# Performance work log

Measured on AMD Instinct MI355X. Metric: run time of the kernel, lower is better.

## Reference

```python
import jax, jax.numpy as jnp
import numpy as np

N_EMBD = 1024
N_HEAD = 16
B, T = 4, 2048
EPS = 1e-5


def setup_inputs() -> dict:
    key = jax.random.key(0)
    ks = jax.random.split(key, 12)
    s = 0.02
    d, dff = N_EMBD, 4 * N_EMBD
    return {
        "x": jax.random.normal(ks[0], (B, T, d), dtype=jnp.float32),
        "ln1_w": jnp.ones((d,), jnp.float32),
        "ln1_b": jnp.zeros((d,), jnp.float32),
        "ln2_w": jnp.ones((d,), jnp.float32),
        "ln2_b": jnp.zeros((d,), jnp.float32),
        "w_attn": jax.random.normal(ks[1], (d, 3 * d), jnp.float32) * s,
        "b_attn": jnp.zeros((3 * d,), jnp.float32),
        "w_proj": jax.random.normal(ks[2], (d, d), jnp.float32) * s,
        "b_proj": jnp.zeros((d,), jnp.float32),
        "w_fc": jax.random.normal(ks[3], (d, dff), jnp.float32) * s,
        "b_fc": jnp.zeros((dff,), jnp.float32),
        "w_fc2": jax.random.normal(ks[4], (dff, d), jnp.float32) * s,
        "b_fc2": jnp.zeros((d,), jnp.float32),
    }


def _layernorm(x, w, b):
    mu = jnp.mean(x, axis=-1, keepdims=True)
    var = jnp.mean(jnp.square(x - mu), axis=-1, keepdims=True)
    return (x - mu) * jax.lax.rsqrt(var + EPS) * w + b


def reference(x, ln1_w, ln1_b, ln2_w, ln2_b, w_attn, b_attn, w_proj, b_proj,
              w_fc, b_fc, w_fc2, b_fc2):
    Bx, Tx, C = x.shape
    hd = C // N_HEAD
    # --- attention branch ---
    h = _layernorm(x, ln1_w, ln1_b)
    qkv = h @ w_attn + b_attn  # [B,T,3C]
    q, k, v = jnp.split(qkv, 3, axis=-1)
    q = q.reshape(Bx, Tx, N_HEAD, hd).transpose(0, 2, 1, 3)  # [B,H,T,hd]
    k = k.reshape(Bx, Tx, N_HEAD, hd).transpose(0, 2, 1, 3)
    v = v.reshape(Bx, Tx, N_HEAD, hd).transpose(0, 2, 1, 3)
    att = jnp.einsum("bhqd,bhkd->bhqk", q, k) * (1.0 / np.sqrt(hd))
    causal = jnp.tril(jnp.ones((Tx, Tx), dtype=bool))
    att = jnp.where(causal[None, None], att, -jnp.inf)
    att = jax.nn.softmax(att, axis=-1)
    y = jnp.einsum("bhqk,bhkd->bhqd", att, v)
    y = y.transpose(0, 2, 1, 3).reshape(Bx, Tx, C)
    x = x + (y @ w_proj + b_proj)
    # --- mlp branch ---
    h2 = _layernorm(x, ln2_w, ln2_b)
    m = jax.nn.gelu(h2 @ w_fc + b_fc, approximate=False)
    x = x + (m @ w_fc2 + b_fc2)
    return x
```

## Files before the change

kernel.cpp:

```cpp
#include <hip/hip_runtime.h>
#include <hip/hip_bf16.h>
#include <math.h>

typedef __bf16 bf16;
typedef __bf16 bf16x4 __attribute__((ext_vector_type(4)));
typedef __bf16 bf16x8 __attribute__((ext_vector_type(8)));
typedef float f32x4 __attribute__((ext_vector_type(4)));

__device__ __forceinline__ void gload_lds16(const bf16* g, bf16* l) {
  __builtin_amdgcn_global_load_lds(
      (const __attribute__((address_space(1))) void*)g,
      (__attribute__((address_space(3))) void*)l, 16, 0, 0);
}

#define MF(a, b, c) __builtin_amdgcn_mfma_f32_16x16x32_bf16((a), (b), (c), 0, 0, 0)
#define VM4_BAR()  asm volatile("s_waitcnt vmcnt(4)\ns_barrier" ::: "memory")
#define VM2_BAR()  asm volatile("s_waitcnt vmcnt(2)\ns_barrier" ::: "memory")
#define VM0_BAR()  asm volatile("s_waitcnt vmcnt(0)\ns_barrier" ::: "memory")
#define LGK0_SB()  do { asm volatile("s_waitcnt lgkmcnt(0)" ::: "memory"); \
                        __builtin_amdgcn_sched_barrier(0); } while (0)

template <int EPI, int KSPLIT>
__global__ __launch_bounds__(512, 2)
void gemmq(const bf16* __restrict__ A, const bf16* __restrict__ BT,
           const float* __restrict__ bias, const float* __restrict__ res,
           void* __restrict__ Cout, void* __restrict__ Cout2,
           int M, int N, int K)
{
  __shared__ alignas(16) bf16 lsA[2][16384];
  __shared__ alignas(16) bf16 lsB[2][16384];

  int nbn = N >> 8;
  int nwg = (M >> 8) * nbn;
  int bid = blockIdx.x;
  int ks = 0;
  if (KSPLIT == 2) { ks = (bid >= nwg) ? 1 : 0; bid -= ks * nwg; }
  int cpx = nwg >> 3;
  int wg  = (bid & 7) * cpx + (bid >> 3);
  int m0 = (wg / nbn) << 8;
  int n0 = (wg % nbn) << 8;

  int t = threadIdx.x;
  int l = t & 63, w = t >> 6;
  int wr = (w >> 2) << 6;
  int wc = (w & 3) << 5;
  int lr = l & 15, lg = l >> 4;

  int kb0 = (KSPLIT == 2) ? ks * (K >> 1) : 0;
  int nt = (K / KSPLIT) >> 6;

  const bf16* Ag = A  + (size_t)m0 * K + kb0;
  const bf16* Bg = BT + (size_t)n0 * K + kb0;

  int swz0 = (lg ^ (lr & 7)) << 3;
  int swz1 = swz0 ^ 32;
  int aRow = (wr + lr) << 6;
  int bRow = (wc + lr) << 6;

  const bf16* srcA[2]; const bf16* srcB[2];
#pragma unroll
  for (int j = 0; j < 2; ++j) {
    int ci = j * 512 + t;
    int r = ci >> 3;
    int g = (ci & 7) ^ (r & 7);
    srcA[j] = Ag + (size_t)r * K + g * 8;
    srcB[j] = Bg + (size_t)r * K + g * 8;
  }
  size_t qA = (size_t)128 * K;

#define STAGE_A(q, kofs, db) do { \
  _Pragma("unroll") \
  for (int j = 0; j < 2; ++j) \
    gload_lds16(srcA[j] + (q) * qA + (kofs), &lsA[db][(q) * 8192 + (j * 512 + t) * 8]); \
} while (0)
#define STAGE_B(q, kofs, db) do { \
  _Pragma("unroll") \
  for (int j = 0; j < 2; ++j) \
    gload_lds16(srcB[j] + (q) * qA + (kofs), &lsB[db][(q) * 8192 + (j * 512 + t) * 8]); \
} while (0)

  f32x4 acc[2][2][4][2];
  f32x4 zero = {0.f, 0.f, 0.f, 0.f};
#pragma unroll
  for (int qa = 0; qa < 2; ++qa)
#pragma unroll
    for (int qb = 0; qb < 2; ++qb)
#pragma unroll
      for (int mi = 0; mi < 4; ++mi)
#pragma unroll
        for (int ni = 0; ni < 2; ++ni) acc[qa][qb][mi][ni] = zero;

  STAGE_A(0, 0, 0);
  STAGE_B(0, 0, 0);
  STAGE_B(1, 0, 0);
  STAGE_A(1, 0, 0);

  bf16x8 afr[4][2], bfr0[2][2], bfr1[2][2];

  for (int T = 0; T < nt; ++T) {
    int c = T & 1, d = c ^ 1;
    bool st = (T + 1 < nt);
    int k64 = (T + 1) << 6;
    const bf16* pa = &lsA[c][0];
    const bf16* pb = &lsB[c][0];

    VM4_BAR();
#pragma unroll
    for (int mi = 0; mi < 4; ++mi) {
      afr[mi][0] = *(const bf16x8*)(pa + aRow + mi * 1024 + swz0);
      afr[mi][1] = *(const bf16x8*)(pa + aRow + mi * 1024 + swz1);
    }
#pragma unroll
    for (int ni = 0; ni < 2; ++ni) {
      bfr0[ni][0] = *(const bf16x8*)(pb + bRow + ni * 1024 + swz0);
      bfr0[ni][1] = *(const bf16x8*)(pb + bRow + ni * 1024 + swz1);
    }
    if (st) STAGE_A(0, k64, d);
    LGK0_SB();
    __builtin_amdgcn_s_setprio(1);
#pragma unroll
    for (int mi = 0; mi < 4; ++mi)
#pragma unroll
      for (int ni = 0; ni < 2; ++ni)
#pragma unroll
        for (int kk = 0; kk < 2; ++kk)
          acc[0][0][mi][ni] = MF(afr[mi][kk], bfr0[ni][kk], acc[0][0][mi][ni]);
    __builtin_amdgcn_s_setprio(0);

    if (st) VM4_BAR(); else VM2_BAR();
#pragma unroll
    for (int ni = 0; ni < 2; ++ni) {
      bfr1[ni][0] = *(const bf16x8*)(pb + 8192 + bRow + ni * 1024 + swz0);
      bfr1[ni][1] = *(const bf16x8*)(pb + 8192 + bRow + ni * 1024 + swz1);
    }
    if (st) STAGE_B(0, k64, d);
    LGK0_SB();
    __builtin_amdgcn_s_setprio(1);
#pragma unroll
    for (int mi = 0; mi < 4; ++mi)
#pragma unroll
      for (int ni = 0; ni < 2; ++ni)
#pragma unroll
        for (int kk = 0; kk < 2; ++kk)
          acc[0][1][mi][ni] = MF(afr[mi][kk], bfr1[ni][kk], acc[0][1][mi][ni]);
    __builtin_amdgcn_s_setprio(0);

    if (st) VM4_BAR(); else VM0_BAR();
#pragma unroll
    for (int mi = 0; mi < 4; ++mi) {
      afr[mi][0] = *(const bf16x8*)(pa + 8192 + aRow + mi * 1024 + swz0);
      afr[mi][1] = *(const bf16x8*)(pa + 8192 + aRow + mi * 1024 + swz1);
    }
    if (st) STAGE_B(1, k64, d);
    LGK0_SB();
    __builtin_amdgcn_s_setprio(1);
#pragma unroll
    for (int mi = 0; mi < 4; ++mi)
#pragma unroll
      for (int ni = 0; ni < 2; ++ni)
#pragma unroll
        for (int kk = 0; kk < 2; ++kk)
          acc[1][1][mi][ni] = MF(afr[mi][kk], bfr1[ni][kk], acc[1][1][mi][ni]);
    __builtin_amdgcn_s_setprio(0);

    if (st) STAGE_A(1, k64, d);
    __builtin_amdgcn_s_setprio(1);
#pragma unroll
    for (int mi = 0; mi < 4; ++mi)
#pragma unroll
      for (int ni = 0; ni < 2; ++ni)
#pragma unroll
        for (int kk = 0; kk < 2; ++kk)
          acc[1][0][mi][ni] = MF(afr[mi][kk], bfr0[ni][kk], acc[1][0][mi][ni]);
    __builtin_amdgcn_s_setprio(0);
  }

  const float SCLQ = 0.18033688011112042f;
  bf16* Pb = (bf16*)((KSPLIT == 2 && ks) ? Cout2 : Cout);
#pragma unroll
  for (int qa = 0; qa < 2; ++qa)
#pragma unroll
    for (int mi = 0; mi < 4; ++mi) {
      int row = m0 + qa * 128 + wr + mi * 16 + lg * 4;
#pragma unroll
      for (int qb = 0; qb < 2; ++qb)
#pragma unroll
        for (int ni = 0; ni < 2; ++ni) {
          int col = n0 + qb * 128 + wc + ni * 16 + lr;
          float bv = (EPI == 3) ? 0.f : bias[col];
          f32x4 a = acc[qa][qb][mi][ni];
#pragma unroll
          for (int r = 0; r < 4; ++r) {
            float v = a[r] + bv;
            size_t idx = (size_t)(row + r) * N + col;
            if (EPI == 0)      Pb[idx] = (bf16)v;
            else if (EPI == 1) ((float*)Cout)[idx] = v + res[idx];
            else if (EPI == 2) Pb[idx] = (bf16)(0.5f * v * (1.f + erff(v * 0.70710678118654752f)));
            else if (EPI == 4) Pb[idx] = (bf16)((col < 1024) ? v * SCLQ : v);
            else               Pb[idx] = (bf16)v;
          }
        }
    }
#undef STAGE_A
#undef STAGE_B
}

__global__ __launch_bounds__(256)
void combine2(const bf16* __restrict__ p0, const bf16* __restrict__ p1,
              const float* __restrict__ bias, const float* __restrict__ res,
              float* __restrict__ out)
{
  int i = (blockIdx.x * 256 + threadIdx.x) * 8;
  bf16x8 a = *(const bf16x8*)(p0 + i);
  bf16x8 b = *(const bf16x8*)(p1 + i);
  int c = i & 1023;
#pragma unroll
  for (int j = 0; j < 8; ++j)
    out[i + j] = (float)a[j] + (float)b[j] + bias[c + j] + res[i + j];
}

__global__ __launch_bounds__(256)
void combine_ln(const bf16* __restrict__ p0, const bf16* __restrict__ p1,
                const float* __restrict__ bias, const float* __restrict__ res,
                const float* __restrict__ lnw, const float* __restrict__ lnb,
                float* __restrict__ x1, bf16* __restrict__ hout)
{
  int row = blockIdx.x;
  int t = threadIdx.x;
  size_t i0 = (size_t)row * 1024 + t * 4;
  bf16x4 a = *(const bf16x4*)(p0 + i0);
  bf16x4 b = *(const bf16x4*)(p1 + i0);
  float4 r = *(const float4*)(res + i0);
  float4 bi = ((const float4*)bias)[t];
  float v0 = (float)a[0] + (float)b[0] + bi.x + r.x;
  float v1 = (float)a[1] + (float)b[1] + bi.y + r.y;
  float v2 = (float)a[2] + (float)b[2] + bi.z + r.z;
  float v3 = (float)a[3] + (float)b[3] + bi.w + r.w;
  float4 vv = {v0, v1, v2, v3};
  *(float4*)(x1 + i0) = vv;
  float s  = v0 + v1 + v2 + v3;
  float sq = v0 * v0 + v1 * v1 + v2 * v2 + v3 * v3;
#pragma unroll
  for (int off = 32; off >= 1; off >>= 1) {
    s  += __shfl_xor(s, off);
    sq += __shfl_xor(sq, off);
  }
  __shared__ float ps[4], pq[4];
  if ((t & 63) == 0) { ps[t >> 6] = s; pq[t >> 6] = sq; }
  __syncthreads();
  s  = ps[0] + ps[1] + ps[2] + ps[3];
  sq = pq[0] + pq[1] + pq[2] + pq[3];
  float mu  = s * (1.f / 1024.f);
  float var = sq * (1.f / 1024.f) - mu * mu;
  float rstd = rsqrtf(var + 1e-5f);
  float4 wv = ((const float4*)lnw)[t];
  float4 bv = ((const float4*)lnb)[t];
  hout[i0 + 0] = (bf16)((v0 - mu) * rstd * wv.x + bv.x);
  hout[i0 + 1] = (bf16)((v1 - mu) * rstd * wv.y + bv.y);
  hout[i0 + 2] = (bf16)((v2 - mu) * rstd * wv.z + bv.z);
  hout[i0 + 3] = (bf16)((v3 - mu) * rstd * wv.w + bv.w);
}

__global__ __launch_bounds__(256)
void ln_bf16(const float* __restrict__ x, const float* __restrict__ w,
             const float* __restrict__ b, bf16* __restrict__ out)
{
  int row = blockIdx.x;
  int t = threadIdx.x;
  float4 v = ((const float4*)(x + (size_t)row * 1024))[t];
  float s  = v.x + v.y + v.z + v.w;
  float sq = v.x * v.x + v.y * v.y + v.z * v.z + v.w * v.w;
#pragma unroll
  for (int off = 32; off >= 1; off >>= 1) {
    s  += __shfl_xor(s, off);
    sq += __shfl_xor(sq, off);
  }
  __shared__ float ps[4], pq[4];
  if ((t & 63) == 0) { ps[t >> 6] = s; pq[t >> 6] = sq; }
  __syncthreads();
  s  = ps[0] + ps[1] + ps[2] + ps[3];
  sq = pq[0] + pq[1] + pq[2] + pq[3];
  float mu  = s * (1.f / 1024.f);
  float var = sq * (1.f / 1024.f) - mu * mu;
  float rstd = rsqrtf(var + 1e-5f);
  float4 wv = ((const float4*)w)[t];
  float4 bv = ((const float4*)b)[t];
  size_t o0 = (size_t)row * 1024 + t * 4;
  out[o0 + 0] = (bf16)((v.x - mu) * rstd * wv.x + bv.x);
  out[o0 + 1] = (bf16)((v.y - mu) * rstd * wv.y + bv.y);
  out[o0 + 2] = (bf16)((v.z - mu) * rstd * wv.z + bv.z);
  out[o0 + 3] = (bf16)((v.w - mu) * rstd * wv.w + bv.w);
}

__global__ __launch_bounds__(256)
void transpose_cast(const float* __restrict__ W, bf16* __restrict__ WT, int K, int N)
{
  __shared__ float tile[32][33];
  int bk = blockIdx.x * 32, bn = blockIdx.y * 32;
  int tx = threadIdx.x & 31, ty = threadIdx.x >> 5;
#pragma unroll
  for (int i = ty; i < 32; i += 8)
    tile[i][tx] = W[(size_t)(bk + i) * N + bn + tx];
  __syncthreads();
#pragma unroll
  for (int i = ty; i < 32; i += 8)
    WT[(size_t)(bn + i) * K + bk + tx] = (bf16)tile[tx][i];
}

__global__ __launch_bounds__(256)
void vtrans(const bf16* __restrict__ qkv, bf16* __restrict__ vt)
{
  __shared__ alignas(16) bf16 tile[64 * 64];
  int bh = blockIdx.x;
  int b = bh >> 4, h = bh & 15;
  int t0 = blockIdx.y * 64;
  int t = threadIdx.x;
#pragma unroll
  for (int i = 0; i < 2; ++i) {
    int c = i * 256 + t;
    int tt = c >> 3, d8 = c & 7;
    bf16x8 v = *(const bf16x8*)(qkv + (size_t)(b * 2048 + t0 + tt) * 3072 + 2048 + h * 64 + d8 * 8);
    *(bf16x8*)&tile[(tt * 8 + (d8 ^ (tt >> 3))) * 8] = v;
  }
  __syncthreads();
#pragma unroll
  for (int i = 0; i < 2; ++i) {
    int c = i * 256 + t;
    int d = c >> 3, tt8 = c & 7;
    bf16x8 o;
#pragma unroll
    for (int j = 0; j < 8; ++j) {
      int row = tt8 * 8 + j;
      o[j] = tile[(row * 8 + ((d >> 3) ^ (row >> 3))) * 8 + (d & 7)];
    }
    *(bf16x8*)(vt + (size_t)(bh * 64 + d) * 2048 + t0 + tt8 * 8) = o;
  }
}

__global__ __launch_bounds__(512)
void attn_flash(const bf16* __restrict__ qkv, const bf16* __restrict__ vt,
                bf16* __restrict__ y)
{
  __shared__ alignas(16) bf16 lk[2][4096];
  __shared__ alignas(16) bf16 lv[2][4096];
  __shared__ alignas(16) bf16 lp[8][16 * 64];

  int bid = blockIdx.x;
  int bh = bid & 63;
  int qb = 15 - (bid >> 6);
  int b = bh >> 4, h = bh & 15;
  int t = threadIdx.x;
  int w = t >> 6, l = t & 63;
  int lr = l & 15, lg = l >> 4;
  int q0 = qb * 128;
  int qw = q0 + w * 16;
  const size_t RS = 3072;

  const bf16* qbase = qkv + (size_t)(b * 2048) * RS + h * 64;
  const bf16* kbase = qkv + (size_t)(b * 2048) * RS + 1024 + h * 64;
  const bf16* vtb   = vt + (size_t)(bh * 64) * 2048;

  bf16x8 qf[2];
#pragma unroll
  for (int kk = 0; kk < 2; ++kk)
    qf[kk] = *(const bf16x8*)(qbase + (size_t)(qw + lr) * RS + kk * 32 + lg * 8);

  int row = t >> 3, c8 = t & 7;
  int sc8 = c8 ^ (row & 7);
  const bf16* pK = kbase + (size_t)row * RS + sc8 * 8;
  const bf16* pV = vtb + (size_t)row * 2048 + sc8 * 8;
  int dst = t * 8;

  f32x4 zero = {0.f, 0.f, 0.f, 0.f};
  f32x4 o[4];
#pragma unroll
  for (int ni = 0; ni < 4; ++ni) o[ni] = zero;
  float lo[4] = {0.f, 0.f, 0.f, 0.f};

  int nkb = 2 * qb + 2;
  gload_lds16(pK, &lk[0][dst]);
  gload_lds16(pV, &lv[0][dst]);

  for (int kb = 0; kb < nkb; ++kb) {
    int cur = kb & 1;
    int k0 = kb * 64;
    VM0_BAR();
    if (kb + 1 < nkb) {
      pK += 64 * RS;
      pV += 64;
      gload_lds16(pK, &lk[cur ^ 1][dst]);
      gload_lds16(pV, &lv[cur ^ 1][dst]);
    }

    f32x4 s[4];
#pragma unroll
    for (int j = 0; j < 4; ++j) s[j] = zero;
#pragma unroll
    for (int kk = 0; kk < 2; ++kk)
#pragma unroll
      for (int j = 0; j < 4; ++j) {
        int krow = j * 16 + lr;
        bf16x8 kf = *(const bf16x8*)&lk[cur][krow * 64 + (((4 * kk + lg) ^ (krow & 7)) * 8)];
        s[j] = MF(qf[kk], kf, s[j]);
      }

    bool needmask = (k0 + 63 > qw);
    float p[4][4];
#pragma unroll
    for (int r = 0; r < 4; ++r) {
      int tq = qw + lg * 4 + r;
#pragma unroll
      for (int j = 0; j < 4; ++j) {
        float v = s[j][r];
        if (needmask && (k0 + j * 16 + lr > tq)) v = -1e30f;
        p[j][r] = exp2f(v);
      }
      lo[r] += (p[0][r] + p[1][r]) + (p[2][r] + p[3][r]);
    }

#pragma unroll
    for (int r = 0; r < 4; ++r) {
      int qr = lg * 4 + r;
#pragma unroll
      for (int j = 0; j < 4; ++j) {
        int ch = (2 * j + (lr >> 3)) ^ (qr & 7);
        lp[w][qr * 64 + ch * 8 + (lr & 7)] = (bf16)p[j][r];
      }
    }
    bf16x8 pa[2];
#pragma unroll
    for (int kf = 0; kf < 2; ++kf)
      pa[kf] = *(const bf16x8*)&lp[w][lr * 64 + (((4 * kf + lg) ^ (lr & 7)) * 8)];

#pragma unroll
    for (int ni = 0; ni < 4; ++ni)
#pragma unroll
      for (int kf = 0; kf < 2; ++kf) {
        int d = ni * 16 + lr;
        bf16x8 vf = *(const bf16x8*)&lv[cur][d * 64 + (((4 * kf + lg) ^ (d & 7)) * 8)];
        o[ni] = MF(pa[kf], vf, o[ni]);
      }
  }

#pragma unroll
  for (int r = 0; r < 4; ++r) {
#pragma unroll
    for (int off = 1; off < 16; off <<= 1) lo[r] += __shfl_xor(lo[r], off);
    lo[r] = 1.f / lo[r];
  }
#pragma unroll
  for (int ni = 0; ni < 4; ++ni)
#pragma unroll
    for (int r = 0; r < 4; ++r) {
      int tq = qw + lg * 4 + r;
      y[(size_t)(b * 2048 + tq) * 1024 + h * 64 + ni * 16 + lr] = (bf16)(o[ni][r] * lo[r]);
    }
}

extern "C" void kernel_launch(void* const* d_in, const int* in_sizes, int n_in,
                              void* d_out, int out_size, void* d_ws, size_t ws_size,
                              hipStream_t stream) {
  (void)in_sizes; (void)n_in; (void)out_size; (void)ws_size;
  const float* x      = (const float*)d_in[0];
  const float* ln1w   = (const float*)d_in[1];
  const float* ln1b   = (const float*)d_in[2];
  const float* ln2w   = (const float*)d_in[3];
  const float* ln2b   = (const float*)d_in[4];
  const float* w_attn = (const float*)d_in[5];
  const float* b_attn = (const float*)d_in[6];
  const float* w_proj = (const float*)d_in[7];
  const float* b_proj = (const float*)d_in[8];
  const float* w_fc   = (const float*)d_in[9];
  const float* b_fc   = (const float*)d_in[10];
  const float* w_fc2  = (const float*)d_in[11];
  const float* b_fc2  = (const float*)d_in[12];
  float* out = (float*)d_out;

  char* p = (char*)d_ws;
  bf16*  h     = (bf16*)p;  p += (size_t)8192 * 1024 * 2;
  bf16*  qkv   = (bf16*)p;
  bf16*  mbuf  = (bf16*)p;  p += (size_t)8192 * 3072 * 2;
  bf16*  ybuf  = (bf16*)p;  p += (size_t)8192 * 1024 * 2;
  float* x1    = (float*)p; p += (size_t)8192 * 1024 * 4;
  bf16*  wqkvT = (bf16*)p;  p += (size_t)3072 * 1024 * 2;
  bf16*  wprojT= (bf16*)p;  p += (size_t)1024 * 1024 * 2;
  bf16*  wfcT  = (bf16*)p;  p += (size_t)4096 * 1024 * 2;
  bf16*  wfc2T = (bf16*)p;  p += (size_t)1024 * 4096 * 2;
  bf16*  vt    = (bf16*)x1;
  bf16*  pp0   = qkv;
  bf16*  pp1   = qkv + (size_t)8192 * 1024;
  bf16*  sp0   = h;
  bf16*  sp1   = wqkvT;

  transpose_cast<<<dim3(1024 / 32, 3072 / 32), 256, 0, stream>>>(w_attn, wqkvT, 1024, 3072);
  transpose_cast<<<dim3(1024 / 32, 1024 / 32), 256, 0, stream>>>(w_proj, wprojT, 1024, 1024);
  transpose_cast<<<dim3(1024 / 32, 4096 / 32), 256, 0, stream>>>(w_fc,   wfcT,  1024, 4096);
  transpose_cast<<<dim3(4096 / 32, 1024 / 32), 256, 0, stream>>>(w_fc2,  wfc2T, 4096, 1024);

  ln_bf16<<<8192, 256, 0, stream>>>(x, ln1w, ln1b, h);
  gemmq<4, 1><<<384, 512, 0, stream>>>(h, wqkvT, b_attn, nullptr, qkv, nullptr, 8192, 3072, 1024);
  vtrans<<<dim3(64, 32), 256, 0, stream>>>(qkv, vt);
  attn_flash<<<1024, 512, 0, stream>>>(qkv, vt, ybuf);
  gemmq<3, 2><<<256, 512, 0, stream>>>(ybuf, wprojT, nullptr, nullptr, pp0, pp1, 8192, 1024, 1024);
  combine_ln<<<8192, 256, 0, stream>>>(pp0, pp1, b_proj, x, ln2w, ln2b, x1, h);
  gemmq<2, 1><<<512, 512, 0, stream>>>(h, wfcT, b_fc, nullptr, mbuf, nullptr, 8192, 4096, 1024);
  gemmq<3, 2><<<256, 512, 0, stream>>>(mbuf, wfc2T, nullptr, nullptr, sp0, sp1, 8192, 1024, 4096);
  combine2<<<4096, 256, 0, stream>>>(sp0, sp1, b_fc2, x1, out);
}
```

Before: 410.9 us.

## Software-pipeline LDS fragment loads across K tiles with register double-buffering

Restructures the GEMM main loop so the first A/B fragments for the next K tile are read from LDS at the end of the current tile, into a second set of registers. The loop is unrolled by two to alternate between the buffer sets. The explicit lgkmcnt(0) waits are replaced by scheduling fences, and the vmcnt thresholds are retuned to the new staging order. This aims to hide LDS read latency behind MFMA work and remove one barrier phase per tile. In exchange it adds VGPR pressure under a 512x2 launch bound, which could cause spills, and it assumes the tile count nt is even.

```diff
diff --git a/kernel.cpp b/kernel.cpp
--- a/kernel.cpp
+++ b/kernel.cpp
@@ -17,8 +17,7 @@
 #define VM4_BAR()  asm volatile("s_waitcnt vmcnt(4)\ns_barrier" ::: "memory")
 #define VM2_BAR()  asm volatile("s_waitcnt vmcnt(2)\ns_barrier" ::: "memory")
 #define VM0_BAR()  asm volatile("s_waitcnt vmcnt(0)\ns_barrier" ::: "memory")
-#define LGK0_SB()  do { asm volatile("s_waitcnt lgkmcnt(0)" ::: "memory"); \
-                        __builtin_amdgcn_sched_barrier(0); } while (0)
+#define SFENCE()   __builtin_amdgcn_sched_barrier(0)
 
 template <int EPI, int KSPLIT>
 __global__ __launch_bounds__(512, 2)
@@ -72,11 +71,13 @@
   _Pragma("unroll") \
   for (int j = 0; j < 2; ++j) \
     gload_lds16(srcA[j] + (q) * qA + (kofs), &lsA[db][(q) * 8192 + (j * 512 + t) * 8]); \
+  SFENCE(); \
 } while (0)
 #define STAGE_B(q, kofs, db) do { \
   _Pragma("unroll") \
   for (int j = 0; j < 2; ++j) \
     gload_lds16(srcB[j] + (q) * qA + (kofs), &lsB[db][(q) * 8192 + (j * 512 + t) * 8]); \
+  SFENCE(); \
 } while (0)
 
   f32x4 acc[2][2][4][2];
@@ -94,85 +95,102 @@
   STAGE_B(0, 0, 0);
   STAGE_B(1, 0, 0);
   STAGE_A(1, 0, 0);
-
-  bf16x8 afr[4][2], bfr0[2][2], bfr1[2][2];
-
-  for (int T = 0; T < nt; ++T) {
-    int c = T & 1, d = c ^ 1;
-    bool st = (T + 1 < nt);
-    int k64 = (T + 1) << 6;
-    const bf16* pa = &lsA[c][0];
-    const bf16* pb = &lsB[c][0];
-
-    VM4_BAR();
-#pragma unroll
-    for (int mi = 0; mi < 4; ++mi) {
-      afr[mi][0] = *(const bf16x8*)(pa + aRow + mi * 1024 + swz0);
-      afr[mi][1] = *(const bf16x8*)(pa + aRow + mi * 1024 + swz1);
-    }
-#pragma unroll
-    for (int ni = 0; ni < 2; ++ni) {
-      bfr0[ni][0] = *(const bf16x8*)(pb + bRow + ni * 1024 + swz0);
-      bfr0[ni][1] = *(const bf16x8*)(pb + bRow + ni * 1024 + swz1);
-    }
-    if (st) STAGE_A(0, k64, d);
-    LGK0_SB();
-    __builtin_amdgcn_s_setprio(1);
-#pragma unroll
-    for (int mi = 0; mi < 4; ++mi)
-#pragma unroll
-      for (int ni = 0; ni < 2; ++ni)
-#pragma unroll
-        for (int kk = 0; kk < 2; ++kk)
-          acc[0][0][mi][ni] = MF(afr[mi][kk], bfr0[ni][kk], acc[0][0][mi][ni]);
-    __builtin_amdgcn_s_setprio(0);
-
-    if (st) VM4_BAR(); else VM2_BAR();
-#pragma unroll
-    for (int ni = 0; ni < 2; ++ni) {
-      bfr1[ni][0] = *(const bf16x8*)(pb + 8192 + bRow + ni * 1024 + swz0);
-      bfr1[ni][1] = *(const bf16x8*)(pb + 8192 + bRow + ni * 1024 + swz1);
-    }
-    if (st) STAGE_B(0, k64, d);
-    LGK0_SB();
-    __builtin_amdgcn_s_setprio(1);
-#pragma unroll
-    for (int mi = 0; mi < 4; ++mi)
-#pragma unroll
-      for (int ni = 0; ni < 2; ++ni)
-#pragma unroll
-        for (int kk = 0; kk < 2; ++kk)
-          acc[0][1][mi][ni] = MF(afr[mi][kk], bfr1[ni][kk], acc[0][1][mi][ni]);
-    __builtin_amdgcn_s_setprio(0);
-
-    if (st) VM4_BAR(); else VM0_BAR();
-#pragma unroll
-    for (int mi = 0; mi < 4; ++mi) {
-      afr[mi][0] = *(const bf16x8*)(pa + 8192 + aRow + mi * 1024 + swz0);
-      afr[mi][1] = *(const bf16x8*)(pa + 8192 + aRow + mi * 1024 + swz1);
-    }
-    if (st) STAGE_B(1, k64, d);
-    LGK0_SB();
-    __builtin_amdgcn_s_setprio(1);
-#pragma unroll
-    for (int mi = 0; mi < 4; ++mi)
-#pragma unroll
-      for (int ni = 0; ni < 2; ++ni)
-#pragma unroll
-        for (int kk = 0; kk < 2; ++kk)
-          acc[1][1][mi][ni] = MF(afr[mi][kk], bfr1[ni][kk], acc[1][1][mi][ni]);
-    __builtin_amdgcn_s_setprio(0);
-
-    if (st) STAGE_A(1, k64, d);
-    __builtin_amdgcn_s_setprio(1);
-#pragma unroll
-    for (int mi = 0; mi < 4; ++mi)
-#pragma unroll
-      for (int ni = 0; ni < 2; ++ni)
-#pragma unroll
-        for (int kk = 0; kk < 2; ++kk)
-          acc[1][0][mi][ni] = MF(afr[mi][kk], bfr0[ni][kk], acc[1][0][mi][ni]);
-    __builtin_amdgcn_s_setprio(0);
+  VM4_BAR();
+
+  bf16x8 a0A[4][2], a0B[4][2], b0A[2][2], b0B[2][2];
+  bf16x8 afr1[4][2], bfr1[2][2];
+
+#pragma unroll
+  for (int mi = 0; mi < 4; ++mi) {
+    a0A[mi][0] = *(const bf16x8*)(&lsA[0][0] + aRow + mi * 1024 + swz0);
+    a0A[mi][1] = *(const bf16x8*)(&lsA[0][0] + aRow + mi * 1024 + swz1);
+  }
+#pragma unroll
+  for (int ni = 0; ni < 2; ++ni) {
+    b0A[ni][0] = *(const bf16x8*)(&lsB[0][0] + bRow + ni * 1024 + swz0);
+    b0A[ni][1] = *(const bf16x8*)(&lsB[0][0] + bRow + ni * 1024 + swz1);
+  }
+
+#define TILE_BODY(TT, CB, A0C, B0C, A0N, B0N) do { \
+  const bf16* pa = &lsA[CB][0]; \
+  const bf16* pb = &lsB[CB][0]; \
+  const int DB = (CB) ^ 1; \
+  bool st = ((TT) + 1 < nt); \
+  int k64 = ((TT) + 1) << 6; \
+   \
+  VM2_BAR(); \
+  _Pragma("unroll") \
+  for (int ni = 0; ni < 2; ++ni) { \
+    bfr1[ni][0] = *(const bf16x8*)(pb + 8192 + bRow + ni * 1024 + swz0); \
+    bfr1[ni][1] = *(const bf16x8*)(pb + 8192 + bRow + ni * 1024 + swz1); \
+  } \
+  if (st) STAGE_A(0, k64, DB); \
+  __builtin_amdgcn_s_setprio(1); \
+  _Pragma("unroll") \
+  for (int mi = 0; mi < 4; ++mi) \
+    _Pragma("unroll") \
+    for (int ni = 0; ni < 2; ++ni) \
+      _Pragma("unroll") \
+      for (int kk = 0; kk < 2; ++kk) \
+        acc[0][0][mi][ni] = MF(A0C[mi][kk], B0C[ni][kk], acc[0][0][mi][ni]); \
+  __builtin_amdgcn_s_setprio(0); \
+   \
+  if (st) VM2_BAR(); else VM0_BAR(); \
+  _Pragma("unroll") \
+  for (int mi = 0; mi < 4; ++mi) { \
+    afr1[mi][0] = *(const bf16x8*)(pa + 8192 + aRow + mi * 1024 + swz0); \
+    afr1[mi][1] = *(const bf16x8*)(pa + 8192 + aRow + mi * 1024 + swz1); \
+  } \
+  if (st) STAGE_B(0, k64, DB); \
+  __builtin_amdgcn_s_setprio(1); \
+  _Pragma("unroll") \
+  for (int mi = 0; mi < 4; ++mi) \
+    _Pragma("unroll") \
+    for (int ni = 0; ni < 2; ++ni) \
+      _Pragma("unroll") \
+      for (int kk = 0; kk < 2; ++kk) \
+        acc[0][1][mi][ni] = MF(A0C[mi][kk], bfr1[ni][kk], acc[0][1][mi][ni]); \
+  __builtin_amdgcn_s_setprio(0); \
+   \
+  if (st) STAGE_B(1, k64, DB); \
+  __builtin_amdgcn_s_setprio(1); \
+  _Pragma("unroll") \
+  for (int mi = 0; mi < 4; ++mi) \
+    _Pragma("unroll") \
+    for (int ni = 0; ni < 2; ++ni) \
+      _Pragma("unroll") \
+      for (int kk = 0; kk < 2; ++kk) \
+        acc[1][1][mi][ni] = MF(afr1[mi][kk], bfr1[ni][kk], acc[1][1][mi][ni]); \
+  __builtin_amdgcn_s_setprio(0); \
+   \
+  if (st) { \
+    VM2_BAR(); \
+    _Pragma("unroll") \
+    for (int mi = 0; mi < 4; ++mi) { \
+      A0N[mi][0] = *(const bf16x8*)(&lsA[DB][0] + aRow + mi * 1024 + swz0); \
+      A0N[mi][1] = *(const bf16x8*)(&lsA[DB][0] + aRow + mi * 1024 + swz1); \
+    } \
+    _Pragma("unroll") \
+    for (int ni = 0; ni < 2; ++ni) { \
+      B0N[ni][0] = *(const bf16x8*)(&lsB[DB][0] + bRow + ni * 1024 + swz0); \
+      B0N[ni][1] = *(const bf16x8*)(&lsB[DB][0] + bRow + ni * 1024 + swz1); \
+    } \
+    STAGE_A(1, k64, DB); \
+  } \
+  __builtin_amdgcn_s_setprio(1); \
+  _Pragma("unroll") \
+  for (int mi = 0; mi < 4; ++mi) \
+    _Pragma("unroll") \
+    for (int ni = 0; ni < 2; ++ni) \
+      _Pragma("unroll") \
+      for (int kk = 0; kk < 2; ++kk) \
+        acc[1][0][mi][ni] = MF(afr1[mi][kk], B0C[ni][kk], acc[1][0][mi][ni]); \
+  __builtin_amdgcn_s_setprio(0); \
+} while (0)
+
+  for (int T = 0; T < nt; T += 2) {
+    TILE_BODY(T,     0, a0A, b0A, a0B, b0B);
+    TILE_BODY(T + 1, 1, a0B, b0B, a0A, b0A);
   }
 
   const float SCLQ = 0.18033688011112042f;
@@ -203,6 +221,7 @@
     }
 #undef STAGE_A
 #undef STAGE_B
+#undef TILE_BODY
 }
 
 __global__ __launch_bounds__(256)
```

After: 997.5 us. 2.43x slower.

## Prefetch next k-tile fragments into registers at end of GEMM iteration

Applied to the files above, without the earlier changes.

Restructures the GEMM main loop so the first A and B fragments of the next k-tile are read from LDS at the end of the current iteration, with a prologue load before the loop. The A fragments now live in two register sets, a0 and afr1. The explicit lgkmcnt(0) waits and sched_barriers are dropped, and the vmcnt barrier thresholds and placement of the global-to-LDS stage issues are reordered. The aim is to hide LDS read latency behind MFMA work. In exchange it raises register pressure under the 512x2 launch bound, adds a barrier per iteration, and depends on the new vmcnt counts being correct.

```diff
diff --git a/kernel.cpp b/kernel.cpp
--- a/kernel.cpp
+++ b/kernel.cpp
@@ -17,8 +17,6 @@
 #define VM4_BAR()  asm volatile("s_waitcnt vmcnt(4)\ns_barrier" ::: "memory")
 #define VM2_BAR()  asm volatile("s_waitcnt vmcnt(2)\ns_barrier" ::: "memory")
 #define VM0_BAR()  asm volatile("s_waitcnt vmcnt(0)\ns_barrier" ::: "memory")
-#define LGK0_SB()  do { asm volatile("s_waitcnt lgkmcnt(0)" ::: "memory"); \
-                        __builtin_amdgcn_sched_barrier(0); } while (0)
 
 template <int EPI, int KSPLIT>
 __global__ __launch_bounds__(512, 2)
@@ -94,8 +92,19 @@
   STAGE_B(0, 0, 0);
   STAGE_B(1, 0, 0);
   STAGE_A(1, 0, 0);
-
-  bf16x8 afr[4][2], bfr0[2][2], bfr1[2][2];
+  VM4_BAR();
+
+  bf16x8 a0[4][2], bfr0[2][2], afr1[4][2], bfr1[2][2];
+#pragma unroll
+  for (int mi = 0; mi < 4; ++mi) {
+    a0[mi][0] = *(const bf16x8*)(&lsA[0][0] + aRow + mi * 1024 + swz0);
+    a0[mi][1] = *(const bf16x8*)(&lsA[0][0] + aRow + mi * 1024 + swz1);
+  }
+#pragma unroll
+  for (int ni = 0; ni < 2; ++ni) {
+    bfr0[ni][0] = *(const bf16x8*)(&lsB[0][0] + bRow + ni * 1024 + swz0);
+    bfr0[ni][1] = *(const bf16x8*)(&lsB[0][0] + bRow + ni * 1024 + swz1);
+  }
 
   for (int T = 0; T < nt; ++T) {
     int c = T & 1, d = c ^ 1;
@@ -104,37 +113,30 @@
     const bf16* pa = &lsA[c][0];
     const bf16* pb = &lsB[c][0];
 
-    VM4_BAR();
-#pragma unroll
-    for (int mi = 0; mi < 4; ++mi) {
-      afr[mi][0] = *(const bf16x8*)(pa + aRow + mi * 1024 + swz0);
-      afr[mi][1] = *(const bf16x8*)(pa + aRow + mi * 1024 + swz1);
-    }
-#pragma unroll
-    for (int ni = 0; ni < 2; ++ni) {
-      bfr0[ni][0] = *(const bf16x8*)(pb + bRow + ni * 1024 + swz0);
-      bfr0[ni][1] = *(const bf16x8*)(pb + bRow + ni * 1024 + swz1);
-    }
-    if (st) STAGE_A(0, k64, d);
-    LGK0_SB();
-    __builtin_amdgcn_s_setprio(1);
-#pragma unroll
-    for (int mi = 0; mi < 4; ++mi)
-#pragma unroll
-      for (int ni = 0; ni < 2; ++ni)
-#pragma unroll
-        for (int kk = 0; kk < 2; ++kk)
-          acc[0][0][mi][ni] = MF(afr[mi][kk], bfr0[ni][kk], acc[0][0][mi][ni]);
-    __builtin_amdgcn_s_setprio(0);
-
-    if (st) VM4_BAR(); else VM2_BAR();
+    VM2_BAR();
 #pragma unroll
     for (int ni = 0; ni < 2; ++ni) {
       bfr1[ni][0] = *(const bf16x8*)(pb + 8192 + bRow + ni * 1024 + swz0);
       bfr1[ni][1] = *(const bf16x8*)(pb + 8192 + bRow + ni * 1024 + swz1);
     }
+    if (st) STAGE_A(0, k64, d);
+    __builtin_amdgcn_s_setprio(1);
+#pragma unroll
+    for (int mi = 0; mi < 4; ++mi)
+#pragma unroll
+      for (int ni = 0; ni < 2; ++ni)
+#pragma unroll
+        for (int kk = 0; kk < 2; ++kk)
+          acc[0][0][mi][ni] = MF(a0[mi][kk], bfr0[ni][kk], acc[0][0][mi][ni]);
+    __builtin_amdgcn_s_setprio(0);
+
+    if (st) VM2_BAR(); else VM0_BAR();
+#pragma unroll
+    for (int mi = 0; mi < 4; ++mi) {
+      afr1[mi][0] = *(const bf16x8*)(pa + 8192 + aRow + mi * 1024 + swz0);
+      afr1[mi][1] = *(const bf16x8*)(pa + 8192 + aRow + mi * 1024 + swz1);
+    }
     if (st) STAGE_B(0, k64, d);
-    LGK0_SB();
     __builtin_amdgcn_s_setprio(1);
 #pragma unroll
     for (int mi = 0; mi < 4; ++mi)
@@ -142,17 +144,10 @@
       for (int ni = 0; ni < 2; ++ni)
 #pragma unroll
         for (int kk = 0; kk < 2; ++kk)
-          acc[0][1][mi][ni] = MF(afr[mi][kk], bfr1[ni][kk], acc[0][1][mi][ni]);
+          acc[0][1][mi][ni] = MF(a0[mi][kk], bfr1[ni][kk], acc[0][1][mi][ni]);
     __builtin_amdgcn_s_setprio(0);
 
-    if (st) VM4_BAR(); else VM0_BAR();
-#pragma unroll
-    for (int mi = 0; mi < 4; ++mi) {
-      afr[mi][0] = *(const bf16x8*)(pa + 8192 + aRow + mi * 1024 + swz0);
-      afr[mi][1] = *(const bf16x8*)(pa + 8192 + aRow + mi * 1024 + swz1);
-    }
     if (st) STAGE_B(1, k64, d);
-    LGK0_SB();
     __builtin_amdgcn_s_setprio(1);
 #pragma unroll
     for (int mi = 0; mi < 4; ++mi)
@@ -160,10 +155,10 @@
       for (int ni = 0; ni < 2; ++ni)
 #pragma unroll
         for (int kk = 0; kk < 2; ++kk)
-          acc[1][1][mi][ni] = MF(afr[mi][kk], bfr1[ni][kk], acc[1][1][mi][ni]);
+          acc[1][1][mi][ni] = MF(afr1[mi][kk], bfr1[ni][kk], acc[1][1][mi][ni]);
     __builtin_amdgcn_s_setprio(0);
 
-    if (st) STAGE_A(1, k64, d);
+    if (st) VM2_BAR();
     __builtin_amdgcn_s_setprio(1);
 #pragma unroll
     for (int mi = 0; mi < 4; ++mi)
@@ -171,8 +166,21 @@
       for (int ni = 0; ni < 2; ++ni)
 #pragma unroll
         for (int kk = 0; kk < 2; ++kk)
-          acc[1][0][mi][ni] = MF(afr[mi][kk], bfr0[ni][kk], acc[1][0][mi][ni]);
+          acc[1][0][mi][ni] = MF(afr1[mi][kk], bfr0[ni][kk], acc[1][0][mi][ni]);
     __builtin_amdgcn_s_setprio(0);
+    if (st) {
+#pragma unroll
+      for (int mi = 0; mi < 4; ++mi) {
+        a0[mi][0] = *(const bf16x8*)(&lsA[d][0] + aRow + mi * 1024 + swz0);
+        a0[mi][1] = *(const bf16x8*)(&lsA[d][0] + aRow + mi * 1024 + swz1);
+      }
+#pragma unroll
+      for (int ni = 0; ni < 2; ++ni) {
+        bfr0[ni][0] = *(const bf16x8*)(&lsB[d][0] + bRow + ni * 1024 + swz0);
+        bfr0[ni][1] = *(const bf16x8*)(&lsB[d][0] + bRow + ni * 1024 + swz1);
+      }
+      STAGE_A(1, k64, d);
+    }
   }
 
   const float SCLQ = 0.18033688011112042f;
```

Measured after the change: 421.1 us. +2.5%, slower.
